# Optimization experiments

Hardware: AMD Instinct MI355X
Metric: run time of the kernel (lower is better)

The kernel has to match this reference:

```python
import jax, jax.numpy as jnp
import numpy as np

HEADS = 16
DIM_HEAD = 64
EPS = 1e-8
MASK_VALUE = -np.finfo(np.float32).max


def rotate_half(x):
    # x: [..., rot_dim]; split into two halves (j=2 grouping) and rotate
    x1, x2 = jnp.split(x.reshape(*x.shape[:-1], 2, x.shape[-1] // 2), 2, axis=-2)
    x1 = x1.squeeze(-2)
    x2 = x2.squeeze(-2)
    return jnp.concatenate((-x2, x1), axis=-1)


def apply_rotary_pos_emb(t, freqs):
    # t: [b, h, n, d], freqs: [n, rot_dim]
    rot_dim = freqs.shape[-1]
    t_rot, t_pass = t[..., :rot_dim], t[..., rot_dim:]
    t_rot = t_rot * jnp.cos(freqs) + rotate_half(t_rot) * jnp.sin(freqs)
    return jnp.concatenate((t_rot, t_pass), axis=-1)


def setup_inputs() -> dict:
    key = jax.random.key(0)
    ks = jax.random.split(key, 6)
    b, n, dim = 2, 2048, 1024
    inner = HEADS * DIM_HEAD
    rot_dim = 32
    return {
        "x": jax.random.normal(ks[0], (b, n, dim), jnp.float32),
        "freqs": jax.random.normal(ks[1], (n, rot_dim), jnp.float32),
        "gamma": jnp.ones((dim,), jnp.float32),
        "Wq": jax.random.normal(ks[2], (dim, inner), jnp.float32) * (dim ** -0.5),
        "Wkv": jax.random.normal(ks[3], (dim, 2 * inner), jnp.float32) * (dim ** -0.5),
        "Wo": jax.random.normal(ks[4], (inner, dim), jnp.float32) * (inner ** -0.5),
        "bo": jnp.zeros((dim,), jnp.float32),
    }


def reference(x, freqs, gamma, Wq, Wkv, Wo, bo):
    b, n, dim = x.shape
    scale = DIM_HEAD ** -0.5

    # RMSNorm (norm-based formulation, matching the torch code)
    norm = jnp.linalg.norm(x, axis=-1, keepdims=True) * (dim ** -0.5)
    xn = x / jnp.maximum(norm, EPS) * gamma

    q = xn @ Wq                      # [b, n, h*d]
    kv = xn @ Wkv                    # [b, n, 2*h*d]
    k, v = jnp.split(kv, 2, axis=-1)

    def to_heads(t):
        return t.reshape(b, n, HEADS, DIM_HEAD).transpose(0, 2, 1, 3)  # [b,h,n,d]

    q, k, v = map(to_heads, (q, k, v))
    q = q * scale

    q = apply_rotary_pos_emb(q, freqs)
    k = apply_rotary_pos_emb(k, freqs)

    sim = jnp.einsum('bhid,bhjd->bhij', q, k)
    causal_mask = jnp.triu(jnp.ones((n, n), bool), k=1)
    sim = jnp.where(causal_mask, MASK_VALUE, sim)

    attn = jax.nn.softmax(sim, axis=-1)
    out = jnp.einsum('bhij,bhjd->bhid', attn, v)
    out = out.transpose(0, 2, 1, 3).reshape(b, n, HEADS * DIM_HEAD)
    return out @ Wo + bo
```

## Files before the change

### kernel.cpp

```cpp
#include <hip/hip_runtime.h>
#include <hip/hip_bf16.h>
#include <math.h>

typedef short s8 __attribute__((ext_vector_type(8)));
typedef float f4 __attribute__((ext_vector_type(4)));

#define HEADS 16
#define DHEAD 64
#define NSEQ 2048
#define BATCH 2
#define DIM 1024
#define ROT 32
#define QSCALE 0.18033688011112042f

static __device__ __forceinline__ unsigned short f2bf(float f) {
    union { float f; unsigned int u; } v; v.f = f;
    unsigned int u = v.u;
    unsigned int r = (u + 0x7FFFu + ((u >> 16) & 1u)) >> 16;
    return (unsigned short)r;
}

static __device__ __forceinline__ unsigned int cvt_pk_bf16(float lo, float hi) {
    unsigned int r;
    asm volatile("v_cvt_pk_bf16_f32 %0, %1, %2" : "=v"(r) : "v"(lo), "v"(hi));
    return r;
}

static __device__ __forceinline__ void gload_lds16(
        const unsigned short* g, unsigned short* l) {
    __builtin_amdgcn_global_load_lds(
        (const __attribute__((address_space(1))) void*)g,
        (__attribute__((address_space(3))) void*)l,
        16, 0, 0);
}

static __device__ __forceinline__ void tr_tile(
        const float* __restrict__ in, unsigned short* __restrict__ out,
        int K, int N, int n0, int k0, int tid, float* tile ) {
    int tx = tid & 31, ty = tid >> 5;
    #pragma unroll
    for (int j = 0; j < 32; j += 8)
        tile[(ty + j) * 33 + tx] = in[(size_t)(k0 + ty + j) * N + n0 + tx];
    __syncthreads();
    #pragma unroll
    for (int j = 0; j < 32; j += 8)
        out[(size_t)(n0 + ty + j) * K + k0 + tx] = f2bf(tile[tx * 33 + ty + j]);
}

__global__ __launch_bounds__(256) void prep_rms_kernel(
        const float* __restrict__ x, const float* __restrict__ gamma,
        const float* __restrict__ Wq, const float* __restrict__ Wkv,
        const float* __restrict__ Wo, const float* __restrict__ freqs,
        unsigned short* __restrict__ xn, unsigned short* __restrict__ WqT,
        unsigned short* __restrict__ WkvT, unsigned short* __restrict__ WoT,
        float* __restrict__ cs) {
    __shared__ float smem[32 * 33];
    int bid = blockIdx.x, tid = threadIdx.x;
    if (bid < 4096) {
        int row = bid;
        float4 v = ((const float4*)(x + (size_t)row * DIM))[tid];
        float ss = v.x * v.x + v.y * v.y + v.z * v.z + v.w * v.w;
        #pragma unroll
        for (int m = 1; m < 64; m <<= 1) ss += __shfl_xor(ss, m, 64);
        int wave = tid >> 6;
        if ((tid & 63) == 0) smem[wave] = ss;
        __syncthreads();
        float total = smem[0] + smem[1] + smem[2] + smem[3];
        float norm = sqrtf(total * (1.0f / DIM));
        float inv = 1.0f / fmaxf(norm, 1e-8f);
        float4 g = ((const float4*)gamma)[tid];
        ushort4 o;
        o.x = f2bf(v.x * inv * g.x);
        o.y = f2bf(v.y * inv * g.y);
        o.z = f2bf(v.z * inv * g.z);
        o.w = f2bf(v.w * inv * g.w);
        ((ushort4*)(xn + (size_t)row * DIM))[tid] = o;
    } else if (bid < 5120) {
        int idx = bid - 4096;
        tr_tile(Wq, WqT, 1024, 1024, (idx & 31) * 32, (idx >> 5) * 32, tid, smem);
    } else if (bid < 7168) {
        int idx = bid - 5120;
        tr_tile(Wkv, WkvT, 1024, 2048, (idx & 63) * 32, (idx >> 6) * 32, tid, smem);
    } else if (bid < 8192) {
        int idx = bid - 7168;
        tr_tile(Wo, WoT, 1024, 1024, (idx & 31) * 32, (idx >> 5) * 32, tid, smem);
    } else {
        int i = (bid - 8192) * 256 + tid;
        int npos = i >> 6, j = i & 63;
        int q = j >> 4;
        int fi = (q >> 1) * 16 + (j & 15);
        float f = freqs[npos * ROT + fi];
        cs[i] = (q & 1) ? sinf(f) : cosf(f);
    }
}

static __device__ __forceinline__ void gemm_core64_p3(
        const unsigned short* __restrict__ A, const unsigned short* __restrict__ BT,
        int bm0, int bn0, unsigned short* As, unsigned short* Bs, f4 acc[2][4]) {
    const int Kd = DIM;
    int tid = threadIdx.x, lane = tid & 63, w = tid >> 6;
    int wr = w >> 1, wc = w & 1;
    int r16 = lane & 15, g8 = 8 * (lane >> 4);
    int srow = lane >> 2, scol = (lane & 3) * 8;
    const unsigned short* Ag0 = A  + (size_t)(bm0 + w * 16 + srow) * Kd + scol;
    const unsigned short* Bg0 = BT + (size_t)(bn0 + (w * 2 + 0) * 16 + srow) * Kd + scol;
    const unsigned short* Bg1 = BT + (size_t)(bn0 + (w * 2 + 1) * 16 + srow) * Kd + scol;
    unsigned short* Al  = As + w * 512;
    unsigned short* Bl0 = Bs + (w * 2 + 0) * 512;
    unsigned short* Bl1 = Bs + (w * 2 + 1) * 512;
    const unsigned short* ar = As + (wr * 32 + r16) * 32 + g8;
    const unsigned short* br = Bs + (wc * 64 + r16) * 32 + g8;
    #pragma unroll
    for (int p = 0; p < 3; ++p) {
        int k0 = p * 32;
        gload_lds16(Ag0 + k0, Al + p * 2048);
        gload_lds16(Bg0 + k0, Bl0 + p * 4096);
        gload_lds16(Bg1 + k0, Bl1 + p * 4096);
    }
    asm volatile("s_waitcnt vmcnt(6)" ::: "memory");
    __builtin_amdgcn_s_barrier();
    __builtin_amdgcn_sched_barrier(0);
    #pragma unroll
    for (int t = 0; t < 32; ++t) {
        const int cb = t % 3;
        const int aoff = cb * 2048;
        const int boff = cb * 4096;
        {
            s8 a0 = *(const s8*)(ar + aoff);
            s8 a1 = *(const s8*)(ar + aoff + 512);
            s8 b0 = *(const s8*)(br + boff);
            s8 b1 = *(const s8*)(br + boff + 512);
            s8 b2 = *(const s8*)(br + boff + 1024);
            s8 b3 = *(const s8*)(br + boff + 1536);
            acc[0][0] = __builtin_amdgcn_mfma_f32_16x16x32_bf16(a0, b0, acc[0][0], 0, 0, 0);
            acc[0][1] = __builtin_amdgcn_mfma_f32_16x16x32_bf16(a0, b1, acc[0][1], 0, 0, 0);
            acc[0][2] = __builtin_amdgcn_mfma_f32_16x16x32_bf16(a0, b2, acc[0][2], 0, 0, 0);
            acc[0][3] = __builtin_amdgcn_mfma_f32_16x16x32_bf16(a0, b3, acc[0][3], 0, 0, 0);
            acc[1][0] = __builtin_amdgcn_mfma_f32_16x16x32_bf16(a1, b0, acc[1][0], 0, 0, 0);
            acc[1][1] = __builtin_amdgcn_mfma_f32_16x16x32_bf16(a1, b1, acc[1][1], 0, 0, 0);
            acc[1][2] = __builtin_amdgcn_mfma_f32_16x16x32_bf16(a1, b2, acc[1][2], 0, 0, 0);
            acc[1][3] = __builtin_amdgcn_mfma_f32_16x16x32_bf16(a1, b3, acc[1][3], 0, 0, 0);
        }
        __builtin_amdgcn_sched_barrier(0);
        __builtin_amdgcn_s_barrier();
        if (t + 3 < 32) {
            int k3 = (t + 3) * 32;
            gload_lds16(Ag0 + k3, Al + aoff);
            gload_lds16(Bg0 + k3, Bl0 + boff);
            gload_lds16(Bg1 + k3, Bl1 + boff);
        }
        if (t + 1 < 32) {
            if (t + 3 < 32)      { asm volatile("s_waitcnt vmcnt(6)" ::: "memory"); }
            else if (t + 2 < 32) { asm volatile("s_waitcnt vmcnt(3)" ::: "memory"); }
            else                 { asm volatile("s_waitcnt vmcnt(0)" ::: "memory"); }
            __builtin_amdgcn_s_barrier();
            __builtin_amdgcn_sched_barrier(0);
        }
    }
}

__global__ __launch_bounds__(256) void gemm_qkv(
        const unsigned short* __restrict__ xn, const unsigned short* __restrict__ WqT,
        const unsigned short* __restrict__ WkvT, const float* __restrict__ cs,
        unsigned short* __restrict__ q_h, unsigned short* __restrict__ k_h,
        unsigned short* __restrict__ v_t) {
    __shared__ unsigned short As[3 * 64 * 32];
    __shared__ unsigned short Bs[3 * 128 * 32];
    f4 acc[2][4];
    #pragma unroll
    for (int m = 0; m < 2; ++m)
        #pragma unroll
        for (int n = 0; n < 4; ++n) acc[m][n] = 0.f;
    int bid = blockIdx.x;
    int xcd = bid & 7;
    int kk = bid >> 3;
    int rx = xcd >> 2, ry = xcd & 3;
    int bx = rx * 12 + (kk % 12);
    int by = ry * 16 + (kk / 12);
    bool isq = (bx < 8);
    int bm0 = by * 64;
    int bn0 = (isq ? bx : (bx - 8)) * 128;
    gemm_core64_p3(xn, isq ? WqT : WkvT, bm0, bn0, As, Bs, acc);
    int tid = threadIdx.x;
    int lane = tid & 63, w = tid >> 6;
    int wr = w >> 1, wc = w & 1, g = lane >> 4, c0 = lane & 15;
    unsigned short* tile = Bs;
    int b_blk = bm0 >> 11;
    int nbase = bm0 & 2047;
    if (isq) {
        #pragma unroll
        for (int m = 0; m < 2; ++m)
            #pragma unroll
            for (int r = 0; r < 4; ++r) {
                int rowl = wr * 32 + m * 16 + 4 * g + r;
                int npos = nbase + rowl;
                const float* csr = cs + npos * 64;
                float a0 = acc[m][0][r] * QSCALE;
                float a1 = acc[m][1][r] * QSCALE;
                float q0 = a0 * csr[c0] - a1 * csr[16 + c0];
                float q1 = a1 * csr[32 + c0] + a0 * csr[48 + c0];
                unsigned short* trow = tile + rowl * 128 + wc * 64;
                trow[c0]      = f2bf(q0);
                trow[16 + c0] = f2bf(q1);
                trow[32 + c0] = f2bf(acc[m][2][r] * QSCALE);
                trow[48 + c0] = f2bf(acc[m][3][r] * QSCALE);
            }
        __syncthreads();
        #pragma unroll
        for (int i = 0; i < 4; ++i) {
            int L = i * 256 + tid;
            int rr = L >> 4, hh = (L >> 3) & 1, ch = L & 7;
            int npos = nbase + rr;
            s8 v = *(const s8*)(tile + rr * 128 + hh * 64 + ch * 8);
            *(s8*)(q_h + ((size_t)(b_blk * HEADS + 2 * bx + hh) * NSEQ + npos) * DHEAD + ch * 8) = v;
        }
    } else if (bx < 16) {
        #pragma unroll
        for (int m = 0; m < 2; ++m)
            #pragma unroll
            for (int r = 0; r < 4; ++r) {
                int rowl = wr * 32 + m * 16 + 4 * g + r;
                int npos = nbase + rowl;
                const float* csr = cs + npos * 64;
                float a0 = acc[m][0][r], a1 = acc[m][1][r];
                float k0v = a0 * csr[c0] - a1 * csr[16 + c0];
                float k1v = a1 * csr[32 + c0] + a0 * csr[48 + c0];
                unsigned short* trow = tile + rowl * 128 + wc * 64;
                trow[c0]      = f2bf(k0v);
                trow[16 + c0] = f2bf(k1v);
                trow[32 + c0] = f2bf(acc[m][2][r]);
                trow[48 + c0] = f2bf(acc[m][3][r]);
            }
        __syncthreads();
        #pragma unroll
        for (int i = 0; i < 4; ++i) {
            int L = i * 256 + tid;
            int rr = L >> 4, hh = (L >> 3) & 1, ch = L & 7;
            int npos = nbase + rr;
            s8 v = *(const s8*)(tile + rr * 128 + hh * 64 + ch * 8);
            *(s8*)(k_h + ((size_t)(b_blk * HEADS + 2 * (bx - 8) + hh) * NSEQ + npos) * DHEAD + ch * 8) = v;
        }
    } else {
        #pragma unroll
        for (int m = 0; m < 2; ++m) {
            int r0 = wr * 32 + m * 16 + 4 * g;
            #pragma unroll
            for (int n = 0; n < 4; ++n) {
                int col = wc * 64 + n * 16 + c0;
                uint2 pk;
                pk.x = cvt_pk_bf16(acc[m][n][0], acc[m][n][1]);
                pk.y = cvt_pk_bf16(acc[m][n][2], acc[m][n][3]);
                *(uint2*)(tile + col * 72 + r0) = pk;
            }
        }
        __syncthreads();
        #pragma unroll
        for (int i = 0; i < 4; ++i) {
            int L = i * 256 + tid;
            int col = L >> 3, ch = L & 7;
            int h = 2 * (bx - 16) + (col >> 6);
            int d = col & 63;
            s8 v = *(const s8*)(tile + col * 72 + ch * 8);
            *(s8*)(v_t + ((size_t)(b_blk * HEADS + h) * DHEAD + d) * NSEQ + nbase + ch * 8) = v;
        }
    }
}


static __device__ __forceinline__ void stage_kv64(
        const unsigned short* __restrict__ kb, const unsigned short* __restrict__ vb,
        int j0, unsigned short* Kd, unsigned short* Vd, int w, int lane) {
    int r8 = lane >> 3, c = lane & 7;
    int sc = c ^ r8;
    #pragma unroll
    for (int i = 0; i < 2; ++i) {
        int rb = (w * 2 + i) * 8;
        int r = rb + r8;
        gload_lds16(kb + (size_t)(j0 + r) * DHEAD + sc * 8, Kd + rb * DHEAD);
        gload_lds16(vb + (size_t)r * NSEQ + j0 + sc * 8,    Vd + rb * DHEAD);
    }
}

template<bool MASKT>
static __device__ __forceinline__ void attn_tile_lds(
        int j0, int q0, int g, int c0, int njt,
        const unsigned short* Kc, const unsigned short* Vc,
        s8 qf0, s8 qf1, unsigned short* plw,
        f4 o[4], float& m, f4& ol) {
    int sw = c0 & 7;
    int off0 = ((g ^ sw) << 3);
    int off1 = (((g + 4) ^ sw) << 3);
    f4 s[4];
    #pragma unroll
    for (int jt = 0; jt < 4; ++jt) {
        f4 acc; acc = 0.f;
        if (!MASKT || jt < njt) {
            const unsigned short* kp = Kc + (jt * 16 + c0) * DHEAD;
            s8 kf0 = *(const s8*)(kp + off0);
            s8 kf1 = *(const s8*)(kp + off1);
            acc = __builtin_amdgcn_mfma_f32_16x16x32_bf16(kf0, qf0, acc, 0, 0, 0);
            acc = __builtin_amdgcn_mfma_f32_16x16x32_bf16(kf1, qf1, acc, 0, 0, 0);
        }
        s[jt] = acc;
    }
    if (MASKT) {
        #pragma unroll
        for (int jt = 0; jt < 4; ++jt)
            #pragma unroll
            for (int r = 0; r < 4; ++r) {
                int j = j0 + jt * 16 + 4 * g + r;
                if (j > q0 + c0) s[jt][r] = -1e30f;
            }
    }
    f4 mv;
    #pragma unroll
    for (int r = 0; r < 4; ++r)
        mv[r] = fmaxf(fmaxf(s[0][r], s[1][r]), fmaxf(s[2][r], s[3][r]));
    float mx = fmaxf(fmaxf(mv[0], mv[1]), fmaxf(mv[2], mv[3]));
    mx = fmaxf(mx, __shfl_xor(mx, 16));
    mx = fmaxf(mx, __shfl_xor(mx, 32));
    if (__any(mx > m + 11.5f)) {
        float mnew = fmaxf(m, mx);
        float alpha = exp2f(m - mnew);
        #pragma unroll
        for (int dc = 0; dc < 4; ++dc)
            #pragma unroll
            for (int r = 0; r < 4; ++r) o[dc][r] *= alpha;
        #pragma unroll
        for (int r = 0; r < 4; ++r) ol[r] *= alpha;
        m = mnew;
    }
    #pragma unroll
    for (int jt = 0; jt < 4; ++jt) {
        f4 p;
        #pragma unroll
        for (int r = 0; r < 4; ++r) p[r] = exp2f(s[jt][r] - m);
        uint2 pk;
        pk.x = cvt_pk_bf16(p[0], p[1]);
        pk.y = cvt_pk_bf16(p[2], p[3]);
        int swc = (2 * jt + (g >> 1)) ^ sw;
        *(uint2*)(plw + c0 * 64 + swc * 8 + (g & 1) * 4) = pk;
    }
    __builtin_amdgcn_sched_barrier(0);
    asm volatile("s_waitcnt lgkmcnt(0)" ::: "memory");
    __builtin_amdgcn_sched_barrier(0);
    s8 pf0 = *(const s8*)(plw + c0 * 64 + ((g ^ sw) << 3));
    s8 pf1 = *(const s8*)(plw + c0 * 64 + (((4 + g) ^ sw) << 3));
    bool hi_half = (!MASKT) || (njt > 2);
    const s8 onesf = {(short)0x3F80, (short)0x3F80, (short)0x3F80, (short)0x3F80,
                      (short)0x3F80, (short)0x3F80, (short)0x3F80, (short)0x3F80};
    ol = __builtin_amdgcn_mfma_f32_16x16x32_bf16(onesf, pf0, ol, 0, 0, 0);
    if (hi_half)
        ol = __builtin_amdgcn_mfma_f32_16x16x32_bf16(onesf, pf1, ol, 0, 0, 0);
    #pragma unroll
    for (int dc = 0; dc < 4; ++dc) {
        const unsigned short* vp = Vc + (dc * 16 + c0) * DHEAD;
        s8 vf0 = *(const s8*)(vp + off0);
        o[dc] = __builtin_amdgcn_mfma_f32_16x16x32_bf16(vf0, pf0, o[dc], 0, 0, 0);
        if (hi_half) {
            s8 vf1 = *(const s8*)(vp + off1);
            o[dc] = __builtin_amdgcn_mfma_f32_16x16x32_bf16(vf1, pf1, o[dc], 0, 0, 0);
        }
    }
}

__global__ __launch_bounds__(256) void attn_kernel(
        const unsigned short* __restrict__ q_h, const unsigned short* __restrict__ k_h,
        const unsigned short* __restrict__ v_t, unsigned short* __restrict__ attn_out) {
    __shared__ unsigned short Ks[2][64 * DHEAD];
    __shared__ unsigned short Vs[2][64 * DHEAD];
    __shared__ unsigned short p_lds[4][16][64];
    int tid = threadIdx.x, lane = tid & 63, w = tid >> 6;
    int g = lane >> 4, c0 = lane & 15;
    int bid = blockIdx.x;
    int k = bid >> 3;
    int qt = 31 - (k >> 2);
    int bh = (bid & 7) + ((k & 3) << 3);
    const unsigned short* qb = q_h + (size_t)bh * NSEQ * DHEAD;
    const unsigned short* kb = k_h + (size_t)bh * NSEQ * DHEAD;
    const unsigned short* vb = v_t + (size_t)bh * DHEAD * NSEQ;
    unsigned short* plw = &p_lds[w][0][0];
    int b = bh >> 4, h = bh & 15;
    int q0 = qt * 64 + w * 16;
    s8 qf0 = *(const s8*)(qb + (size_t)(q0 + c0) * DHEAD + 8 * g);
    s8 qf1 = *(const s8*)(qb + (size_t)(q0 + c0) * DHEAD + 32 + 8 * g);
    f4 o[4]; o[0] = 0.f; o[1] = 0.f; o[2] = 0.f; o[3] = 0.f;
    f4 ol; ol = 0.f;
    float m = -1e30f;
    int nt = qt + 1;
    stage_kv64(kb, vb, 0, Ks[0], Vs[0], w, lane);
    __syncthreads();
    for (int t = 0; t < nt; ++t) {
        const unsigned short* Kc = Ks[t & 1];
        const unsigned short* Vc = Vs[t & 1];
        if (t + 1 < nt)
            stage_kv64(kb, vb, (t + 1) * 64, Ks[(t + 1) & 1], Vs[(t + 1) & 1], w, lane);
        if (t == nt - 1)
            attn_tile_lds<true>(t * 64, q0, g, c0, w + 1, Kc, Vc, qf0, qf1, plw, o, m, ol);
        else
            attn_tile_lds<false>(t * 64, q0, g, c0, 4, Kc, Vc, qf0, qf1, plw, o, m, ol);
        __syncthreads();
    }
    float invl = 1.0f / ol[0];
    unsigned short* dst = attn_out + ((size_t)(b * NSEQ) + q0 + c0) * (HEADS * DHEAD) + h * DHEAD;
    #pragma unroll
    for (int dc = 0; dc < 4; ++dc) {
        uint2 pk;
        pk.x = cvt_pk_bf16(o[dc][0] * invl, o[dc][1] * invl);
        pk.y = cvt_pk_bf16(o[dc][2] * invl, o[dc][3] * invl);
        *(uint2*)(dst + dc * 16 + 4 * g) = pk;
    }
}

__global__ __launch_bounds__(256) void gemm_o(
        const unsigned short* __restrict__ attn, const unsigned short* __restrict__ WoT,
        const float* __restrict__ bo, float* __restrict__ out) {
    __shared__ unsigned short As[3 * 64 * 32];
    __shared__ unsigned short Bs[3 * 128 * 32];
    __shared__ float tileF[64 * 132];
    f4 acc[2][4];
    #pragma unroll
    for (int m = 0; m < 2; ++m)
        #pragma unroll
        for (int n = 0; n < 4; ++n) acc[m][n] = 0.f;
    int bid = blockIdx.x;
    int xcd = bid & 7;
    int kk = bid >> 3;
    int bx = kk & 7;
    int by = xcd * 8 + (kk >> 3);
    int bm0 = by * 64, bn0 = bx * 128;
    gemm_core64_p3(attn, WoT, bm0, bn0, As, Bs, acc);
    int tid = threadIdx.x;
    int lane = tid & 63, w = tid >> 6;
    int wr = w >> 1, wc = w & 1, g = lane >> 4, c0 = lane & 15;
    #pragma unroll
    for (int m = 0; m < 2; ++m)
        #pragma unroll
        for (int r = 0; r < 4; ++r) {
            int rowl = wr * 32 + m * 16 + 4 * g + r;
            #pragma unroll
            for (int n = 0; n < 4; ++n) {
                int col_l = wc * 64 + n * 16 + c0;
                tileF[rowl * 132 + col_l] = acc[m][n][r] + bo[bn0 + col_l];
            }
        }
    __syncthreads();
    #pragma unroll
    for (int i = 0; i < 8; ++i) {
        int L = i * 256 + tid;
        int rr = L >> 5, ch = L & 31;
        f4 v = *(const f4*)(tileF + rr * 132 + ch * 4);
        *(f4*)(out + (size_t)(bm0 + rr) * DIM + bn0 + ch * 4) = v;
    }
}

extern "C" void kernel_launch(void* const* d_in, const int* in_sizes, int n_in,
                              void* d_out, int out_size, void* d_ws, size_t ws_size,
                              hipStream_t stream) {
    const float* x     = (const float*)d_in[0];
    const float* freqs = (const float*)d_in[1];
    const float* gamma = (const float*)d_in[2];
    const float* Wq    = (const float*)d_in[3];
    const float* Wkv   = (const float*)d_in[4];
    const float* Wo    = (const float*)d_in[5];
    const float* bo    = (const float*)d_in[6];
    float* out = (float*)d_out;

    char* ws = (char*)d_ws;
    unsigned short* xn   = (unsigned short*)(ws + 0);
    unsigned short* WqT  = (unsigned short*)(ws + 8388608);
    unsigned short* WkvT = (unsigned short*)(ws + 10485760);
    unsigned short* WoT  = (unsigned short*)(ws + 14680064);
    unsigned short* q_h  = (unsigned short*)(ws + 16777216);
    unsigned short* k_h  = (unsigned short*)(ws + 25165824);
    unsigned short* v_t  = (unsigned short*)(ws + 33554432);
    float*          cs   = (float*)(ws + 41943040);
    unsigned short* attn = xn;

    prep_rms_kernel<<<8704, 256, 0, stream>>>(x, gamma, Wq, Wkv, Wo, freqs,
                                              xn, WqT, WkvT, WoT, cs);
    gemm_qkv<<<1536, 256, 0, stream>>>(xn, WqT, WkvT, cs, q_h, k_h, v_t);
    attn_kernel<<<1024, 256, 0, stream>>>(q_h, k_h, v_t, attn);
    gemm_o  <<<512, 256, 0, stream>>>(attn, WoT, bo, out);
}
```

Before: 124.6 us.

## Shrink attention KV tile from 64 to 32 keys with per-wave causal skipping

The attention inner loop now stages and processes 32-key tiles instead of 64, halving K/V/P shared memory. Each wave skips tiles entirely above its causal boundary and applies the mask only on its own diagonal tile. This is meant to cut wasted masked work and LDS footprint, which may raise occupancy. The cost is twice as many loop iterations, each with its own barrier and online-softmax max/rescale step, and less MFMA work per synchronization.

```diff
diff --git a/kernel.cpp b/kernel.cpp
--- a/kernel.cpp
+++ b/kernel.cpp
@@ -11,6 +11,7 @@
 #define BATCH 2
 #define DIM 1024
 #define ROT 32
+#define KVB 32
 #define QSCALE 0.18033688011112042f
 
 static __device__ __forceinline__ unsigned short f2bf(float f) {
@@ -267,45 +268,41 @@
 }
 
 
-static __device__ __forceinline__ void stage_kv64(
+static __device__ __forceinline__ void stage_kv32(
         const unsigned short* __restrict__ kb, const unsigned short* __restrict__ vb,
         int j0, unsigned short* Kd, unsigned short* Vd, int w, int lane) {
-    int r8 = lane >> 3, c = lane & 7;
-    int sc = c ^ r8;
-    #pragma unroll
-    for (int i = 0; i < 2; ++i) {
-        int rb = (w * 2 + i) * 8;
-        int r = rb + r8;
-        gload_lds16(kb + (size_t)(j0 + r) * DHEAD + sc * 8, Kd + rb * DHEAD);
-        gload_lds16(vb + (size_t)r * NSEQ + j0 + sc * 8,    Vd + rb * DHEAD);
-    }
+    int r8 = lane >> 3, c8 = lane & 7;
+    int sck = c8 ^ r8;
+    gload_lds16(kb + (size_t)(j0 + w * 8 + r8) * DHEAD + sck * 8, Kd + (w * 8) * DHEAD);
+    int r4 = lane >> 2, c4 = lane & 3;
+    int rowv = w * 16 + r4;
+    int scv = c4 ^ (r4 & 3);
+    gload_lds16(vb + (size_t)rowv * NSEQ + j0 + scv * 8, Vd + (w * 16) * KVB);
 }
 
 template<bool MASKT>
-static __device__ __forceinline__ void attn_tile_lds(
-        int j0, int q0, int g, int c0, int njt,
+static __device__ __forceinline__ void attn_tile32(
+        int j0, int q0, int g, int c0,
         const unsigned short* Kc, const unsigned short* Vc,
         s8 qf0, s8 qf1, unsigned short* plw,
         f4 o[4], float& m, f4& ol) {
     int sw = c0 & 7;
     int off0 = ((g ^ sw) << 3);
     int off1 = (((g + 4) ^ sw) << 3);
-    f4 s[4];
-    #pragma unroll
-    for (int jt = 0; jt < 4; ++jt) {
+    f4 s[2];
+    #pragma unroll
+    for (int jt = 0; jt < 2; ++jt) {
         f4 acc; acc = 0.f;
-        if (!MASKT || jt < njt) {
-            const unsigned short* kp = Kc + (jt * 16 + c0) * DHEAD;
-            s8 kf0 = *(const s8*)(kp + off0);
-            s8 kf1 = *(const s8*)(kp + off1);
-            acc = __builtin_amdgcn_mfma_f32_16x16x32_bf16(kf0, qf0, acc, 0, 0, 0);
-            acc = __builtin_amdgcn_mfma_f32_16x16x32_bf16(kf1, qf1, acc, 0, 0, 0);
-        }
+        const unsigned short* kp = Kc + (jt * 16 + c0) * DHEAD;
+        s8 kf0 = *(const s8*)(kp + off0);
+        s8 kf1 = *(const s8*)(kp + off1);
+        acc = __builtin_amdgcn_mfma_f32_16x16x32_bf16(kf0, qf0, acc, 0, 0, 0);
+        acc = __builtin_amdgcn_mfma_f32_16x16x32_bf16(kf1, qf1, acc, 0, 0, 0);
         s[jt] = acc;
     }
     if (MASKT) {
         #pragma unroll
-        for (int jt = 0; jt < 4; ++jt)
+        for (int jt = 0; jt < 2; ++jt)
             #pragma unroll
             for (int r = 0; r < 4; ++r) {
                 int j = j0 + jt * 16 + 4 * g + r;
@@ -314,8 +311,7 @@
     }
     f4 mv;
     #pragma unroll
-    for (int r = 0; r < 4; ++r)
-        mv[r] = fmaxf(fmaxf(s[0][r], s[1][r]), fmaxf(s[2][r], s[3][r]));
+    for (int r = 0; r < 4; ++r) mv[r] = fmaxf(s[0][r], s[1][r]);
     float mx = fmaxf(fmaxf(mv[0], mv[1]), fmaxf(mv[2], mv[3]));
     mx = fmaxf(mx, __shfl_xor(mx, 16));
     mx = fmaxf(mx, __shfl_xor(mx, 32));
@@ -330,46 +326,39 @@
         for (int r = 0; r < 4; ++r) ol[r] *= alpha;
         m = mnew;
     }
-    #pragma unroll
-    for (int jt = 0; jt < 4; ++jt) {
+    int swp = c0 & 3;
+    #pragma unroll
+    for (int jt = 0; jt < 2; ++jt) {
         f4 p;
         #pragma unroll
         for (int r = 0; r < 4; ++r) p[r] = exp2f(s[jt][r] - m);
         uint2 pk;
         pk.x = cvt_pk_bf16(p[0], p[1]);
         pk.y = cvt_pk_bf16(p[2], p[3]);
-        int swc = (2 * jt + (g >> 1)) ^ sw;
-        *(uint2*)(plw + c0 * 64 + swc * 8 + (g & 1) * 4) = pk;
+        int swc = (2 * jt + (g >> 1)) ^ swp;
+        *(uint2*)(plw + c0 * KVB + swc * 8 + (g & 1) * 4) = pk;
     }
     __builtin_amdgcn_sched_barrier(0);
     asm volatile("s_waitcnt lgkmcnt(0)" ::: "memory");
     __builtin_amdgcn_sched_barrier(0);
-    s8 pf0 = *(const s8*)(plw + c0 * 64 + ((g ^ sw) << 3));
-    s8 pf1 = *(const s8*)(plw + c0 * 64 + (((4 + g) ^ sw) << 3));
-    bool hi_half = (!MASKT) || (njt > 2);
+    s8 pf = *(const s8*)(plw + c0 * KVB + ((g ^ swp) << 3));
     const s8 onesf = {(short)0x3F80, (short)0x3F80, (short)0x3F80, (short)0x3F80,
                       (short)0x3F80, (short)0x3F80, (short)0x3F80, (short)0x3F80};
-    ol = __builtin_amdgcn_mfma_f32_16x16x32_bf16(onesf, pf0, ol, 0, 0, 0);
-    if (hi_half)
-        ol = __builtin_amdgcn_mfma_f32_16x16x32_bf16(onesf, pf1, ol, 0, 0, 0);
+    ol = __builtin_amdgcn_mfma_f32_16x16x32_bf16(onesf, pf, ol, 0, 0, 0);
     #pragma unroll
     for (int dc = 0; dc < 4; ++dc) {
-        const unsigned short* vp = Vc + (dc * 16 + c0) * DHEAD;
-        s8 vf0 = *(const s8*)(vp + off0);
-        o[dc] = __builtin_amdgcn_mfma_f32_16x16x32_bf16(vf0, pf0, o[dc], 0, 0, 0);
-        if (hi_half) {
-            s8 vf1 = *(const s8*)(vp + off1);
-            o[dc] = __builtin_amdgcn_mfma_f32_16x16x32_bf16(vf1, pf1, o[dc], 0, 0, 0);
-        }
+        const unsigned short* vp = Vc + (dc * 16 + c0) * KVB + ((g ^ swp) << 3);
+        s8 vf = *(const s8*)(vp);
+        o[dc] = __builtin_amdgcn_mfma_f32_16x16x32_bf16(vf, pf, o[dc], 0, 0, 0);
     }
 }
 
 __global__ __launch_bounds__(256) void attn_kernel(
         const unsigned short* __restrict__ q_h, const unsigned short* __restrict__ k_h,
         const unsigned short* __restrict__ v_t, unsigned short* __restrict__ attn_out) {
-    __shared__ unsigned short Ks[2][64 * DHEAD];
-    __shared__ unsigned short Vs[2][64 * DHEAD];
-    __shared__ unsigned short p_lds[4][16][64];
+    __shared__ unsigned short Ks[2][KVB * DHEAD];
+    __shared__ unsigned short Vs[2][DHEAD * KVB];
+    __shared__ unsigned short p_lds[4][16][KVB];
     int tid = threadIdx.x, lane = tid & 63, w = tid >> 6;
     int g = lane >> 4, c0 = lane & 15;
     int bid = blockIdx.x;
@@ -387,18 +376,19 @@
     f4 o[4]; o[0] = 0.f; o[1] = 0.f; o[2] = 0.f; o[3] = 0.f;
     f4 ol; ol = 0.f;
     float m = -1e30f;
-    int nt = qt + 1;
-    stage_kv64(kb, vb, 0, Ks[0], Vs[0], w, lane);
+    int nt = 2 * qt + 2;
+    int tmask = 2 * qt + (w >> 1);
+    stage_kv32(kb, vb, 0, Ks[0], Vs[0], w, lane);
     __syncthreads();
     for (int t = 0; t < nt; ++t) {
         const unsigned short* Kc = Ks[t & 1];
         const unsigned short* Vc = Vs[t & 1];
         if (t + 1 < nt)
-            stage_kv64(kb, vb, (t + 1) * 64, Ks[(t + 1) & 1], Vs[(t + 1) & 1], w, lane);
-        if (t == nt - 1)
-            attn_tile_lds<true>(t * 64, q0, g, c0, w + 1, Kc, Vc, qf0, qf1, plw, o, m, ol);
-        else
-            attn_tile_lds<false>(t * 64, q0, g, c0, 4, Kc, Vc, qf0, qf1, plw, o, m, ol);
+            stage_kv32(kb, vb, (t + 1) * KVB, Ks[(t + 1) & 1], Vs[(t + 1) & 1], w, lane);
+        if (t < tmask)
+            attn_tile32<false>(t * KVB, q0, g, c0, Kc, Vc, qf0, qf1, plw, o, m, ol);
+        else if (t == tmask)
+            attn_tile32<true>(t * KVB, q0, g, c0, Kc, Vc, qf0, qf1, plw, o, m, ol);
         __syncthreads();
     }
     float invl = 1.0f / ol[0];
```

Result: slower. 145.1 us (+16.4%).
